# Optimization experiments

Hardware: AMD Instinct MI355X
Metric: run time of the kernel (lower is better)

The kernel has to match this reference:

```python
import jax, jax.numpy as jnp
import numpy as np

N, E, D, H, C = 50000, 800000, 128, 4, 32  # nodes, edges, in/out dim, heads, head dim
NEG_SLOPE = 0.2
LN_EPS = 1e-5
NORM_EPS = 1e-12


def setup_inputs() -> dict:
    key = jax.random.key(0)
    ks = jax.random.split(key, 10)
    s = 1.0 / np.sqrt(D)
    return {
        "x": jax.random.normal(ks[0], (N, D), dtype=jnp.float32),
        "edge_index": jax.random.randint(ks[1], (2, E), 0, N, dtype=jnp.int64),
        "gamma": 1.0 + 0.1 * jax.random.normal(ks[2], (D,), dtype=jnp.float32),
        "beta": 0.1 * jax.random.normal(ks[3], (D,), dtype=jnp.float32),
        "W_l": jax.random.normal(ks[4], (D, H * C), dtype=jnp.float32) * s,
        "b_l": jnp.zeros((H * C,), dtype=jnp.float32),
        "W_r": jax.random.normal(ks[5], (D, H * C), dtype=jnp.float32) * s,
        "b_r": jnp.zeros((H * C,), dtype=jnp.float32),
        "att": jax.random.normal(ks[6], (H, C), dtype=jnp.float32) * s,
        "bias": jnp.zeros((H * C,), dtype=jnp.float32),
        "scale": jnp.array(1.0, dtype=jnp.float32),
    }


def reference(x, edge_index, gamma, beta, W_l, b_l, W_r, b_r, att, bias, scale):
    n = x.shape[0]
    # Pre-activation: LayerNorm -> ReLU (dropout=0 in eval)
    mu = jnp.mean(x, axis=-1, keepdims=True)
    var = jnp.mean(jnp.square(x - mu), axis=-1, keepdims=True)
    h = jax.nn.relu((x - mu) / jnp.sqrt(var + LN_EPS) * gamma + beta)

    # GATv2Conv (PyG defaults: add_self_loops=True, negative_slope=0.2)
    loops = jnp.arange(n, dtype=edge_index.dtype)
    src = jnp.concatenate([edge_index[0], loops])  # message source j
    dst = jnp.concatenate([edge_index[1], loops])  # message target i

    xl = (h @ W_l + b_l).reshape(n, H, C)
    xr = (h @ W_r + b_r).reshape(n, H, C)

    # per-edge GATv2 score: a^T LeakyReLU(xl[j] + xr[i])  -> [E2, H]
    feat = jax.nn.leaky_relu(xl[src] + xr[dst], NEG_SLOPE)
    e = jnp.einsum('ehc,hc->eh', feat, att)

    # segment softmax over incoming edges of each target node
    m = jax.ops.segment_max(e, dst, num_segments=n)
    p = jnp.exp(e - m[dst])
    denom = jax.ops.segment_sum(p, dst, num_segments=n)
    alpha = p / denom[dst]  # [E2, H]

    # scatter-aggregate weighted source features
    msg = alpha[:, :, None] * xl[src]  # [E2, H, C]
    out = jax.ops.segment_sum(msg, dst, num_segments=n).reshape(n, H * C) + bias

    # MsgNorm: normalize(msg) * ||h||_2 * scale
    out_norm = jnp.sqrt(jnp.sum(jnp.square(out), axis=-1, keepdims=True))
    msg_n = out / jnp.maximum(out_norm, NORM_EPS)
    h_norm = jnp.sqrt(jnp.sum(jnp.square(h), axis=-1, keepdims=True))
    gat_out = msg_n * h_norm * scale

    # residual (projection is None since in_channels == out_channels)
    return x + gat_out
```

## Files before the change

### kernel.cpp

```cpp
#include <hip/hip_runtime.h>
#include <hip/hip_bf16.h>
#include <math.h>

#define N_NODES 50000
#define N_EDGES 800000
#define E2 (N_EDGES + N_NODES)
#define D 128

#define NB_LN 12500
#define NB_W 128

#define BSHIFT 8
#define NBUCK 196
#define SCHUNK 4096
#define NB_SC ((E2 + SCHUNK - 1) / SCHUNK)
#define NB_GEMM (((N_NODES + 127) / 128) * 2)

typedef short short8 __attribute__((ext_vector_type(8)));
typedef float f32x4 __attribute__((ext_vector_type(4)));
typedef _Float16 h16x2 __attribute__((ext_vector_type(2)));
typedef _Float16 h16x8 __attribute__((ext_vector_type(8)));

__device__ __forceinline__ float waveReduceSum(float v) {
#pragma unroll
  for (int off = 32; off >= 1; off >>= 1) v += __shfl_xor(v, off);
  return v;
}

__device__ __forceinline__ h16x2 shfl_xor_h2(h16x2 v, int off) {
  int r = __shfl_xor(__builtin_bit_cast(int, v), off);
  return __builtin_bit_cast(h16x2, r);
}

__global__ void __launch_bounds__(256) k_pre(
    const float* __restrict__ x, const float* __restrict__ gamma,
    const float* __restrict__ beta, const float* __restrict__ Wl,
    const float* __restrict__ Wr, const int* __restrict__ ei,
    __hip_bfloat16* __restrict__ hb, float* __restrict__ hnorm,
    __hip_bfloat16* __restrict__ Wt, int* __restrict__ bcnt) {
  const int b = blockIdx.x;
  if (b < NB_LN) {
    int wid = threadIdx.x >> 6;
    int lane = threadIdx.x & 63;
    int i = b * 4 + wid;
    const float2 xv = *(const float2*)&x[(size_t)i * D + lane * 2];
    float s = waveReduceSum(xv.x + xv.y);
    float mean = s * (1.0f / D);
    float d0 = xv.x - mean, d1 = xv.y - mean;
    float vs = waveReduceSum(d0 * d0 + d1 * d1);
    float rstd = rsqrtf(vs * (1.0f / D) + 1e-5f);
    const float2 g = *(const float2*)&gamma[lane * 2];
    const float2 bb = *(const float2*)&beta[lane * 2];
    float h0 = fmaxf(d0 * rstd * g.x + bb.x, 0.0f);
    float h1 = fmaxf(d1 * rstd * g.y + bb.y, 0.0f);
    __hip_bfloat162 hv;
    hv.x = __float2bfloat16(h0);
    hv.y = __float2bfloat16(h1);
    *(__hip_bfloat162*)&hb[(size_t)i * D + lane * 2] = hv;
    float ns = waveReduceSum(h0 * h0 + h1 * h1);
    if (lane == 0) hnorm[i] = sqrtf(ns);
  } else if (b < NB_LN + NB_W) {
    int local = b - NB_LN;
    int n = local * 2 + (threadIdx.x >> 7);
    int k = threadIdx.x & 127;
    float v = (n < D) ? Wl[(size_t)k * D + n] : Wr[(size_t)k * D + (n - D)];
    Wt[n * D + k] = __float2bfloat16(v);
  } else {
    __shared__ int c[256];
    const int t = threadIdx.x;
    c[t] = 0;
    __syncthreads();
    const int s0 = (b - NB_LN - NB_W) * SCHUNK;
#pragma unroll
    for (int k = 0; k < 16; ++k) {
      int e = s0 + t + k * 256;
      if (e < E2) {
        int dst = (e < N_EDGES) ? ei[N_EDGES + e] : (e - N_EDGES);
        atomicAdd(&c[dst >> BSHIFT], 1);
      }
    }
    __syncthreads();
    if (c[t]) atomicAdd(&bcnt[t], c[t]);
  }
}

__global__ void __launch_bounds__(256) k_bscatter(const int* __restrict__ ei,
                                                  const int* __restrict__ bcnt,
                                                  int* __restrict__ cnt0,
                                                  int2* __restrict__ bucketed) {
  __shared__ int c[256], base[256], sd[256];
  const int t = threadIdx.x;
  const int own = (t < NBUCK) ? bcnt[t] : 0;
  sd[t] = own;
  c[t] = 0;
  __syncthreads();
  for (int off = 1; off < 256; off <<= 1) {
    int u = 0;
    if (t >= off) u = sd[t - off];
    __syncthreads();
    if (t >= off) sd[t] += u;
    __syncthreads();
  }
  const int boffL = sd[t] - own;
  const int s0 = blockIdx.x * SCHUNK;
#pragma unroll
  for (int k = 0; k < 16; ++k) {
    int e = s0 + t + k * 256;
    if (e < E2) {
      int dst = (e < N_EDGES) ? ei[N_EDGES + e] : (e - N_EDGES);
      atomicAdd(&c[dst >> BSHIFT], 1);
    }
  }
  __syncthreads();
  if (t < NBUCK) {
    base[t] = c[t] ? (boffL + atomicAdd(&cnt0[t], c[t])) : 0;
    c[t] = 0;
  }
  __syncthreads();
#pragma unroll
  for (int k = 0; k < 16; ++k) {
    int e = s0 + t + k * 256;
    if (e < E2) {
      int src, dst;
      if (e < N_EDGES) {
        src = ei[e];
        dst = ei[N_EDGES + e];
      } else {
        src = dst = e - N_EDGES;
      }
      int bk = dst >> BSHIFT;
      int pos = base[bk] + atomicAdd(&c[bk], 1);
      bucketed[pos] = make_int2(src, dst);
    }
  }
}

__global__ void __launch_bounds__(256) k_mid(
    const int2* __restrict__ bucketed, const int* __restrict__ bcnt,
    int* __restrict__ rowptr, int* __restrict__ csr,
    const __hip_bfloat16* __restrict__ hb, const __hip_bfloat16* __restrict__ Wt,
    const float* __restrict__ bL, const float* __restrict__ bR,
    _Float16* __restrict__ xlh, _Float16* __restrict__ xrh) {
  __shared__ char smem[65536];
  const int t = threadIdx.x;
  if (blockIdx.x < NBUCK) {
    int* cnt = (int*)smem;
    int* tsum = cnt + 256;
    int* cursor = tsum + 256;
    int* red = cursor + 256;
    const int b = blockIdx.x;
    const int base = b << BSHIFT;
    const int nnode = min(256, N_NODES - base);
    red[t] = (t < b) ? bcnt[t] : 0;
    cnt[t] = 0;
    __syncthreads();
    for (int off = 128; off >= 1; off >>= 1) {
      if (t < off) red[t] += red[t + off];
      __syncthreads();
    }
    const int e0 = red[0], e1 = red[0] + bcnt[b];
    if (b == 0) {
      if (t == 0) rowptr[N_NODES] = E2;
      if (t < 32) csr[E2 + t] = 0;
    }
    for (int e = e0 + t; e < e1; e += 256) {
      int2 pr = bucketed[e];
      atomicAdd(&cnt[pr.y - base], 1);
    }
    __syncthreads();
    const int own = cnt[t];
    tsum[t] = own;
    __syncthreads();
    for (int off = 1; off < 256; off <<= 1) {
      int u = 0;
      if (t >= off) u = tsum[t - off];
      __syncthreads();
      if (t >= off) tsum[t] += u;
      __syncthreads();
    }
    const int ebase = e0 + tsum[t] - own;
    cursor[t] = ebase;
    if (t < nnode) rowptr[base + t] = ebase;
    __syncthreads();
    for (int e = e0 + t; e < e1; e += 256) {
      int2 pr = bucketed[e];
      int pos = atomicAdd(&cursor[pr.y - base], 1);
      csr[pos] = pr.x;
    }
  } else {
    unsigned short* As = (unsigned short*)smem;
    unsigned short* Bs = As + 128 * 128;
    const int bid = blockIdx.x - NBUCK;
    const int row0 = (bid >> 1) * 128;
    const int nhalf = bid & 1;
    const unsigned short* hu = (const unsigned short*)hb;
    const unsigned short* wu = (const unsigned short*)Wt;
#pragma unroll
    for (int it = 0; it < 8; ++it) {
      int idx = t + it * 256;
      int r = idx >> 4, g = idx & 15;
      int gs = g ^ (r & 15);
      short8 av = {};
      int grow = row0 + r;
      if (grow < N_NODES) av = *(const short8*)&hu[(size_t)grow * D + g * 8];
      *(short8*)&As[r * 128 + gs * 8] = av;
      short8 bv = *(const short8*)&wu[(size_t)(nhalf * 128 + r) * D + g * 8];
      *(short8*)&Bs[r * 128 + gs * 8] = bv;
    }
    __syncthreads();
    const int w = t >> 6, lane = t & 63;
    const int wm = (w >> 1) * 64, wn = (w & 1) * 64;
    const int lr = lane & 15, lq = lane >> 4;
    f32x4 acc[4][4] = {};
#pragma unroll
    for (int kb = 0; kb < 4; ++kb) {
      short8 af[4], bfr[4];
#pragma unroll
      for (int mi = 0; mi < 4; ++mi) {
        int r = wm + mi * 16 + lr;
        int g = (kb * 4 + lq) ^ (r & 15);
        af[mi] = *(const short8*)&As[r * 128 + g * 8];
      }
#pragma unroll
      for (int ni = 0; ni < 4; ++ni) {
        int r = wn + ni * 16 + lr;
        int g = (kb * 4 + lq) ^ (r & 15);
        bfr[ni] = *(const short8*)&Bs[r * 128 + g * 8];
      }
#pragma unroll
      for (int mi = 0; mi < 4; ++mi)
#pragma unroll
        for (int ni = 0; ni < 4; ++ni)
          acc[mi][ni] = __builtin_amdgcn_mfma_f32_16x16x32_bf16(af[mi], bfr[ni],
                                                                acc[mi][ni], 0, 0, 0);
    }
    const float* bb = (nhalf == 0) ? bL : bR;
    _Float16* dst = (nhalf == 0) ? xlh : xrh;
#pragma unroll
    for (int mi = 0; mi < 4; ++mi) {
#pragma unroll
      for (int ni = 0; ni < 4; ++ni) {
#pragma unroll
        for (int r = 0; r < 4; ++r) {
          int row = row0 + wm + mi * 16 + lq * 4 + r;
          int col = wn + ni * 16 + lr;
          if (row < N_NODES)
            dst[(size_t)row * D + col] = (_Float16)(acc[mi][ni][r] + bb[col]);
        }
      }
    }
  }
}

__global__ void __launch_bounds__(256) k_node(
    const float* __restrict__ x, const _Float16* __restrict__ xlh,
    const _Float16* __restrict__ xrh, const float* __restrict__ hnorm,
    const int* __restrict__ rowptr, const int* __restrict__ csr,
    const float* __restrict__ att, const float* __restrict__ bias,
    const float* __restrict__ scale, float* __restrict__ out) {
  const int wid = threadIdx.x >> 6;
  const int lane = threadIdx.x & 63;
  const int i = blockIdx.x * 4 + wid;
  if (i >= N_NODES) return;
  const int g = lane >> 4;
  const int q = lane & 15;

  const h16x8 xrv = *(const h16x8*)(xrh + (size_t)i * D + q * 8);
  h16x2 xr2[4], at2[4];
  {
    const float LOG2E = 1.44269504f;
    const float4 a0 = *(const float4*)&att[q * 8];
    const float4 a1 = *(const float4*)&att[q * 8 + 4];
    at2[0] = (h16x2){(_Float16)(a0.x * LOG2E), (_Float16)(a0.y * LOG2E)};
    at2[1] = (h16x2){(_Float16)(a0.z * LOG2E), (_Float16)(a0.w * LOG2E)};
    at2[2] = (h16x2){(_Float16)(a1.x * LOG2E), (_Float16)(a1.y * LOG2E)};
    at2[3] = (h16x2){(_Float16)(a1.z * LOG2E), (_Float16)(a1.w * LOG2E)};
#pragma unroll
    for (int z = 0; z < 4; ++z) xr2[z] = (h16x2){xrv[2 * z], xrv[2 * z + 1]};
  }
  const h16x2 c02 = {(_Float16)0.2f, (_Float16)0.2f};

  const int e0 = rowptr[i], e1 = rowptr[i + 1];
  h16x2 A2[4] = {};
  float S = 0.f;

  int ja = csr[e0 + g];
  h16x8 r0 = *(const h16x8*)(xlh + (size_t)ja * D + q * 8);
  int jb = csr[e0 + 4 + g];
  h16x8 r1 = *(const h16x8*)(xlh + (size_t)jb * D + q * 8);
  int jc = csr[e0 + 8 + g];
  h16x8 r2 = *(const h16x8*)(xlh + (size_t)jc * D + q * 8);
  int jd = csr[e0 + 12 + g];

  for (int e = e0; e < e1; e += 4) {
    const h16x8 cur = r0;
    r0 = r1;
    r1 = r2;
    r2 = *(const h16x8*)(xlh + (size_t)jd * D + q * 8);
    jd = csr[e + 16 + g];
    const bool ok = (e + g) < e1;

    h16x2 v2[4];
    v2[0] = (h16x2){cur[0], cur[1]};
    v2[1] = (h16x2){cur[2], cur[3]};
    v2[2] = (h16x2){cur[4], cur[5]};
    v2[3] = (h16x2){cur[6], cur[7]};
    float sc = 0.f;
#pragma unroll
    for (int z = 0; z < 4; ++z) {
      h16x2 f = v2[z] + xr2[z];
      h16x2 lf = __builtin_elementwise_max(f, f * c02);
      sc = __builtin_amdgcn_fdot2(lf, at2[z], sc, false);
    }
    sc += __shfl_xor(sc, 1);
    sc += __shfl_xor(sc, 2);
    const float p = ok ? __builtin_exp2f(sc) : 0.f;
    S += p;
    const _Float16 ph = (_Float16)p;
    const h16x2 p2 = {ph, ph};
#pragma unroll
    for (int z = 0; z < 4; ++z) A2[z] = v2[z] * p2 + A2[z];
  }

#pragma unroll
  for (int off = 16; off <= 32; off <<= 1) {
#pragma unroll
    for (int z = 0; z < 4; ++z) A2[z] = A2[z] + shfl_xor_h2(A2[z], off);
    S += __shfl_xor(S, off);
  }

  const float si = 1.0f / S;
  float o[8];
  float b8[8];
  *(float4*)&b8[0] = *(const float4*)&bias[q * 8];
  *(float4*)&b8[4] = *(const float4*)&bias[q * 8 + 4];
  float dot = 0.f;
#pragma unroll
  for (int z = 0; z < 4; ++z) {
    o[2 * z] = fmaf((float)A2[z][0], si, b8[2 * z]);
    o[2 * z + 1] = fmaf((float)A2[z][1], si, b8[2 * z + 1]);
    dot = fmaf(o[2 * z], o[2 * z], dot);
    dot = fmaf(o[2 * z + 1], o[2 * z + 1], dot);
  }
  const float nrm = sqrtf(waveReduceSum(dot) * 0.25f);
  const float gg = hnorm[i] * scale[0] / fmaxf(nrm, 1e-12f);

  if (lane < 16) {
    float x8[8];
    *(float4*)&x8[0] = *(const float4*)&x[(size_t)i * D + q * 8];
    *(float4*)&x8[4] = *(const float4*)&x[(size_t)i * D + q * 8 + 4];
    float r8[8];
#pragma unroll
    for (int z = 0; z < 8; ++z) r8[z] = fmaf(o[z], gg, x8[z]);
    *(float4*)&out[(size_t)i * D + q * 8] = *(float4*)&r8[0];
    *(float4*)&out[(size_t)i * D + q * 8 + 4] = *(float4*)&r8[4];
  }
}

extern "C" void kernel_launch(void* const* d_in, const int* in_sizes, int n_in,
                              void* d_out, int out_size, void* d_ws, size_t ws_size,
                              hipStream_t stream) {
  const float* x = (const float*)d_in[0];
  const int* ei = (const int*)d_in[1];
  const float* gamma = (const float*)d_in[2];
  const float* beta = (const float*)d_in[3];
  const float* Wl = (const float*)d_in[4];
  const float* bL = (const float*)d_in[5];
  const float* Wr = (const float*)d_in[6];
  const float* bR = (const float*)d_in[7];
  const float* att = (const float*)d_in[8];
  const float* bias = (const float*)d_in[9];
  const float* scale = (const float*)d_in[10];
  float* out = (float*)d_out;

  int2* bucketed = (int2*)d_ws;
  int* csr = (int*)(bucketed + E2);
  int* rowptr = csr + E2 + 32;
  int* bcnt = rowptr + N_NODES + 16;
  int* cnt0 = bcnt + 256;
  float* hnorm = (float*)(cnt0 + 256);
  __hip_bfloat16* hb = (__hip_bfloat16*)(hnorm + N_NODES);
  __hip_bfloat16* Wt = hb + (size_t)N_NODES * D;
  _Float16* xlh = (_Float16*)(Wt + 256 * D);
  _Float16* xrh = xlh + (size_t)N_NODES * D;

  hipMemsetAsync(bcnt, 0, 512 * sizeof(int), stream);
  k_pre<<<NB_LN + NB_W + NB_SC, 256, 0, stream>>>(x, gamma, beta, Wl, Wr, ei, hb,
                                                  hnorm, Wt, bcnt);
  k_bscatter<<<NB_SC, 256, 0, stream>>>(ei, bcnt, cnt0, bucketed);
  k_mid<<<NBUCK + NB_GEMM, 256, 0, stream>>>(bucketed, bcnt, rowptr, csr, hb, Wt,
                                             bL, bR, xlh, xrh);
  k_node<<<(N_NODES + 3) / 4, 256, 0, stream>>>(x, xlh, xrh, hnorm, rowptr, csr, att,
                                                bias, scale, out);
}
```

Measured before the change: 117.9 us.

## Map one node per 16-lane group in aggregation kernel instead of per wave

The node aggregation kernel now assigns each 16-lane quarter-wave its own target node, so a wave handles four nodes rather than splitting one node's edges across four groups. Each group walks its own edge list for the wave's maximum degree and masks out the extra iterations. This drops the cross-group shuffle reduction of the accumulators and the idle lanes in the epilogue, and launches a quarter as many blocks. In exchange, divergent degrees within a wave waste iterations, the serial per-group edge chain is longer, and the csr padding grows to 64 to cover the prefetch overrun. The bounds check was removed, which relies on the node count being a multiple of 16.

After: 119.9 us. Within noise of the previous version (+1.7%).

```diff
diff --git a/kernel.cpp b/kernel.cpp
--- a/kernel.cpp
+++ b/kernel.cpp
@@ -25,11 +25,6 @@
 #pragma unroll
   for (int off = 32; off >= 1; off >>= 1) v += __shfl_xor(v, off);
   return v;
-}
-
-__device__ __forceinline__ h16x2 shfl_xor_h2(h16x2 v, int off) {
-  int r = __shfl_xor(__builtin_bit_cast(int, v), off);
-  return __builtin_bit_cast(h16x2, r);
 }
 
 __global__ void __launch_bounds__(256) k_pre(
@@ -161,7 +156,7 @@
     const int e0 = red[0], e1 = red[0] + bcnt[b];
     if (b == 0) {
       if (t == 0) rowptr[N_NODES] = E2;
-      if (t < 32) csr[E2 + t] = 0;
+      if (t < 64) csr[E2 + t] = 0;
     }
     for (int e = e0 + t; e < e1; e += 256) {
       int2 pr = bucketed[e];
@@ -260,10 +255,9 @@
     const float* __restrict__ scale, float* __restrict__ out) {
   const int wid = threadIdx.x >> 6;
   const int lane = threadIdx.x & 63;
-  const int i = blockIdx.x * 4 + wid;
-  if (i >= N_NODES) return;
   const int g = lane >> 4;
   const int q = lane & 15;
+  const int i = blockIdx.x * 16 + wid * 4 + g;
 
   const h16x8 xrv = *(const h16x8*)(xrh + (size_t)i * D + q * 8);
   h16x2 xr2[4], at2[4];
@@ -281,24 +275,29 @@
   const h16x2 c02 = {(_Float16)0.2f, (_Float16)0.2f};
 
   const int e0 = rowptr[i], e1 = rowptr[i + 1];
+  const int deg = e1 - e0;
+  int maxdeg = deg;
+  maxdeg = max(maxdeg, __shfl_xor(maxdeg, 16));
+  maxdeg = max(maxdeg, __shfl_xor(maxdeg, 32));
+
   h16x2 A2[4] = {};
   float S = 0.f;
 
-  int ja = csr[e0 + g];
+  int ja = csr[e0];
   h16x8 r0 = *(const h16x8*)(xlh + (size_t)ja * D + q * 8);
-  int jb = csr[e0 + 4 + g];
+  int jb = csr[e0 + 1];
   h16x8 r1 = *(const h16x8*)(xlh + (size_t)jb * D + q * 8);
-  int jc = csr[e0 + 8 + g];
+  int jc = csr[e0 + 2];
   h16x8 r2 = *(const h16x8*)(xlh + (size_t)jc * D + q * 8);
-  int jd = csr[e0 + 12 + g];
-
-  for (int e = e0; e < e1; e += 4) {
+  int jd = csr[e0 + 3];
+
+  for (int it = 0; it < maxdeg; ++it) {
     const h16x8 cur = r0;
     r0 = r1;
     r1 = r2;
     r2 = *(const h16x8*)(xlh + (size_t)jd * D + q * 8);
-    jd = csr[e + 16 + g];
-    const bool ok = (e + g) < e1;
+    jd = csr[e0 + it + 4];
+    const bool ok = it < deg;
 
     h16x2 v2[4];
     v2[0] = (h16x2){cur[0], cur[1]};
@@ -322,13 +321,6 @@
     for (int z = 0; z < 4; ++z) A2[z] = v2[z] * p2 + A2[z];
   }
 
-#pragma unroll
-  for (int off = 16; off <= 32; off <<= 1) {
-#pragma unroll
-    for (int z = 0; z < 4; ++z) A2[z] = A2[z] + shfl_xor_h2(A2[z], off);
-    S += __shfl_xor(S, off);
-  }
-
   const float si = 1.0f / S;
   float o[8];
   float b8[8];
@@ -342,19 +334,19 @@
     dot = fmaf(o[2 * z], o[2 * z], dot);
     dot = fmaf(o[2 * z + 1], o[2 * z + 1], dot);
   }
-  const float nrm = sqrtf(waveReduceSum(dot) * 0.25f);
+#pragma unroll
+  for (int off = 8; off >= 1; off >>= 1) dot += __shfl_xor(dot, off, 16);
+  const float nrm = sqrtf(dot);
   const float gg = hnorm[i] * scale[0] / fmaxf(nrm, 1e-12f);
 
-  if (lane < 16) {
-    float x8[8];
-    *(float4*)&x8[0] = *(const float4*)&x[(size_t)i * D + q * 8];
-    *(float4*)&x8[4] = *(const float4*)&x[(size_t)i * D + q * 8 + 4];
-    float r8[8];
-#pragma unroll
-    for (int z = 0; z < 8; ++z) r8[z] = fmaf(o[z], gg, x8[z]);
-    *(float4*)&out[(size_t)i * D + q * 8] = *(float4*)&r8[0];
-    *(float4*)&out[(size_t)i * D + q * 8 + 4] = *(float4*)&r8[4];
-  }
+  float x8[8];
+  *(float4*)&x8[0] = *(const float4*)&x[(size_t)i * D + q * 8];
+  *(float4*)&x8[4] = *(const float4*)&x[(size_t)i * D + q * 8 + 4];
+  float r8[8];
+#pragma unroll
+  for (int z = 0; z < 8; ++z) r8[z] = fmaf(o[z], gg, x8[z]);
+  *(float4*)&out[(size_t)i * D + q * 8] = *(float4*)&r8[0];
+  *(float4*)&out[(size_t)i * D + q * 8 + 4] = *(float4*)&r8[4];
 }
 
 extern "C" void kernel_launch(void* const* d_in, const int* in_sizes, int n_in,
@@ -375,7 +367,7 @@
 
   int2* bucketed = (int2*)d_ws;
   int* csr = (int*)(bucketed + E2);
-  int* rowptr = csr + E2 + 32;
+  int* rowptr = csr + E2 + 64;
   int* bcnt = rowptr + N_NODES + 16;
   int* cnt0 = bcnt + 256;
   float* hnorm = (float*)(cnt0 + 256);
@@ -390,6 +382,6 @@
   k_bscatter<<<NB_SC, 256, 0, stream>>>(ei, bcnt, cnt0, bucketed);
   k_mid<<<NBUCK + NB_GEMM, 256, 0, stream>>>(bucketed, bcnt, rowptr, csr, hb, Wt,
                                              bL, bR, xlh, xrh);
-  k_node<<<(N_NODES + 3) / 4, 256, 0, stream>>>(x, xlh, xrh, hnorm, rowptr, csr, att,
-                                                bias, scale, out);
-}
+  k_node<<<N_NODES / 16, 256, 0, stream>>>(x, xlh, xrh, hnorm, rowptr, csr, att,
+                                           bias, scale, out);
+}
```
